# Performance work log

Hardware: AMD Instinct MI355X
Metric: run time of the kernel (lower is better)

Reference implementation:

```python
import jax, jax.numpy as jnp
import numpy as np

EPS = 1e-8  # torch.nn.CosineSimilarity default eps


def setup_inputs() -> dict:
    key = jax.random.key(0)
    k1, k2, k3 = jax.random.split(key, 3)
    B, T, D, L = 16, 256, 512, 32
    v1 = jax.random.normal(k1, (B, T, D), dtype=jnp.float32)
    v1_mask = jnp.ones((B, T), dtype=jnp.float32)
    v2 = jax.random.normal(k2, (B, D), dtype=jnp.float32)
    w = jax.random.normal(k3, (L, D), dtype=jnp.float32)
    return {"v1": v1, "v1_mask": v1_mask, "v2": v2, "w": w}


def reference(v1, v1_mask, v2, w):
    # v1: [B,T,D], v1_mask: [B,T], v2: [B,D], w: [L,D]
    # Original math: cos over D of (w * v1) and (w * v2), per perspective l.
    # Fused: (w_l*a)\cdot(w_l*b) = sum_d w[l,d]^2 a[d] b[d]; likewise for norms.
    v1m = v1 * v1_mask[:, :, None]              # [B,T,D]
    w2 = w * w                                   # [L,D]
    num = jnp.einsum('btd,ld,bd->btl', v1m, w2, v2)          # [B,T,L]
    n1 = jnp.sqrt(jnp.einsum('btd,ld->btl', v1m * v1m, w2))  # [B,T,L]
    n2 = jnp.sqrt(jnp.einsum('bd,ld->bl', v2 * v2, w2))      # [B,L]
    denom = jnp.maximum(n1 * n2[:, None, :], EPS)
    return num / denom                           # [B,T,L]
```

## Files before the change

### kernel.cpp

```cpp
#include <hip/hip_runtime.h>
#include <cstddef>

#define BB      16
#define TDIM    256
#define DDIM    512
#define LDIM    32
#define TROWS   16
#define CD      128
#define NCHUNK  (DDIM / CD)
#define EPSV    1e-8f

__global__ __launch_bounds__(256, 1) void fullmatch_kernel(
    const float* __restrict__ v1,
    const float* __restrict__ v1_mask,
    const float* __restrict__ v2,
    const float* __restrict__ w,
    float* __restrict__ out)
{
    const int tid  = threadIdx.x;
    const int b    = blockIdx.x >> 4;
    const int tgrp = blockIdx.x & 15;
    const int t0b  = tgrp * TROWS;

    const int l  = tid & 31;
    const int tg = tid >> 5;
    const int t0 = t0b + tg * 2;

    __shared__ float v1s[TROWS][CD];
    __shared__ float ws[LDIM][CD + 1];
    __shared__ float hs[LDIM][CD + 1];
    __shared__ float n2s[LDIM];
    __shared__ float red[8][LDIM];

    const float* v2b = v2 + (size_t)b * DDIM;

    {
        const float* wrow = w + (size_t)l * DDIM + tg * 64;
        const float* vseg = v2b + tg * 64;
        float acc = 0.f;
        #pragma unroll 8
        for (int i = 0; i < 64; ++i) {
            const float wv = wrow[i];
            const float vv = vseg[i];
            acc = fmaf(wv * wv, vv * vv, acc);
        }
        red[tg][l] = acc;
    }
    __syncthreads();
    if (tid < LDIM) {
        float s = 0.f;
        #pragma unroll
        for (int i = 0; i < 8; ++i) s += red[i][tid];
        n2s[tid] = sqrtf(s);
    }

    float num0 = 0.f, num1 = 0.f, n1a = 0.f, n1b = 0.f;

    for (int c = 0; c < NCHUNK; ++c) {
        const int d0 = c * CD;
        __syncthreads();

        #pragma unroll
        for (int k = 0; k < 2; ++k) {
            const int f = tid + k * 256;
            const int r = f >> 5;
            const int q = f & 31;
            const float4 val = *(const float4*)(v1 + (size_t)(b * TDIM + t0b + r) * DDIM + d0 + q * 4);
            const float  mk  = v1_mask[b * TDIM + t0b + r];
            float4 o;
            o.x = val.x * mk; o.y = val.y * mk; o.z = val.z * mk; o.w = val.w * mk;
            *(float4*)(&v1s[r][q * 4]) = o;
        }
        #pragma unroll
        for (int k = 0; k < 4; ++k) {
            const int f = tid + k * 256;
            const int r = f >> 5;
            const int q = f & 31;
            const float4 wv = *(const float4*)(w + (size_t)r * DDIM + d0 + q * 4);
            const float4 vv = *(const float4*)(v2b + d0 + q * 4);
            const float w2x = wv.x * wv.x, w2y = wv.y * wv.y, w2z = wv.z * wv.z, w2w = wv.w * wv.w;
            ws[r][q*4+0] = w2x;        ws[r][q*4+1] = w2y;
            ws[r][q*4+2] = w2z;        ws[r][q*4+3] = w2w;
            hs[r][q*4+0] = w2x * vv.x; hs[r][q*4+1] = w2y * vv.y;
            hs[r][q*4+2] = w2z * vv.z; hs[r][q*4+3] = w2w * vv.w;
        }
        __syncthreads();

        const float* __restrict__ a0p = &v1s[tg * 2][0];
        const float* __restrict__ a1p = &v1s[tg * 2 + 1][0];
        const float* __restrict__ wp  = &ws[l][0];
        const float* __restrict__ hp  = &hs[l][0];

        #pragma unroll 8
        for (int dd = 0; dd < CD; dd += 4) {
            const float4 a0 = *(const float4*)(a0p + dd);
            const float4 a1 = *(const float4*)(a1p + dd);
            const float w0 = wp[dd+0], w1 = wp[dd+1], w2_ = wp[dd+2], w3 = wp[dd+3];
            const float h0 = hp[dd+0], h1 = hp[dd+1], h2  = hp[dd+2], h3 = hp[dd+3];

            num0 = fmaf(a0.x, h0, num0);
            num0 = fmaf(a0.y, h1, num0);
            num0 = fmaf(a0.z, h2, num0);
            num0 = fmaf(a0.w, h3, num0);
            num1 = fmaf(a1.x, h0, num1);
            num1 = fmaf(a1.y, h1, num1);
            num1 = fmaf(a1.z, h2, num1);
            num1 = fmaf(a1.w, h3, num1);

            n1a = fmaf(a0.x * a0.x, w0,  n1a);
            n1a = fmaf(a0.y * a0.y, w1,  n1a);
            n1a = fmaf(a0.z * a0.z, w2_, n1a);
            n1a = fmaf(a0.w * a0.w, w3,  n1a);
            n1b = fmaf(a1.x * a1.x, w0,  n1b);
            n1b = fmaf(a1.y * a1.y, w1,  n1b);
            n1b = fmaf(a1.z * a1.z, w2_, n1b);
            n1b = fmaf(a1.w * a1.w, w3,  n1b);
        }
    }

    const float n2v = n2s[l];
    const float den0 = fmaxf(sqrtf(n1a) * n2v, EPSV);
    const float den1 = fmaxf(sqrtf(n1b) * n2v, EPSV);
    out[(size_t)(b * TDIM + t0)     * LDIM + l] = num0 / den0;
    out[(size_t)(b * TDIM + t0 + 1) * LDIM + l] = num1 / den1;
}

extern "C" void kernel_launch(void* const* d_in, const int* in_sizes, int n_in,
                              void* d_out, int out_size, void* d_ws, size_t ws_size,
                              hipStream_t stream) {
    const float* v1      = (const float*)d_in[0];
    const float* v1_mask = (const float*)d_in[1];
    const float* v2      = (const float*)d_in[2];
    const float* w       = (const float*)d_in[3];
    float* out           = (float*)d_out;

    const dim3 grid(BB * (TDIM / TROWS));
    const dim3 block(256);
    fullmatch_kernel<<<grid, block, 0, stream>>>(v1, v1_mask, v2, w, out);
}
```

Measured before the change: 24.25 us.

## Split D across lanes with register-held weights and shuffle reductions

Each 1024-thread block now loads its full 16x512 v1 tile into shared memory once and gives each of the 32 perspectives one wavefront-half. Each lane keeps w^2 and w^2*v2 for its slice of D in registers, accumulates all 16 rows, and then reduces across lanes with xor shuffles. The aim is to drop the chunked shared staging of w and h, the repeated barriers, and the redundant per-block n2 pass, and to write output as coalesced float4 stores. In exchange each thread holds 32 accumulators, and the block does five shuffle rounds per value plus the larger block-size occupancy trade-offs.

```diff
diff --git a/kernel.cpp b/kernel.cpp
--- a/kernel.cpp
+++ b/kernel.cpp
@@ -6,11 +6,10 @@
 #define DDIM    512
 #define LDIM    32
 #define TROWS   16
-#define CD      128
-#define NCHUNK  (DDIM / CD)
+#define NTHREADS 1024
 #define EPSV    1e-8f
 
-__global__ __launch_bounds__(256, 1) void fullmatch_kernel(
+__global__ __launch_bounds__(NTHREADS, 1) void fullmatch_kernel(
     const float* __restrict__ v1,
     const float* __restrict__ v1_mask,
     const float* __restrict__ v2,
@@ -22,107 +21,97 @@
     const int tgrp = blockIdx.x & 15;
     const int t0b  = tgrp * TROWS;
 
-    const int l  = tid & 31;
-    const int tg = tid >> 5;
-    const int t0 = t0b + tg * 2;
+    const int dq = tid & 31;
+    const int l  = tid >> 5;
 
-    __shared__ float v1s[TROWS][CD];
-    __shared__ float ws[LDIM][CD + 1];
-    __shared__ float hs[LDIM][CD + 1];
-    __shared__ float n2s[LDIM];
-    __shared__ float red[8][LDIM];
+    __shared__ float v1s[TROWS][DDIM];
+    __shared__ float otile[TROWS][LDIM];
 
-    const float* v2b = v2 + (size_t)b * DDIM;
-
+    float4 w2r[4], hr[4];
+    float n2p = 0.f;
     {
-        const float* wrow = w + (size_t)l * DDIM + tg * 64;
-        const float* vseg = v2b + tg * 64;
-        float acc = 0.f;
-        #pragma unroll 8
-        for (int i = 0; i < 64; ++i) {
-            const float wv = wrow[i];
-            const float vv = vseg[i];
-            acc = fmaf(wv * wv, vv * vv, acc);
-        }
-        red[tg][l] = acc;
-    }
-    __syncthreads();
-    if (tid < LDIM) {
-        float s = 0.f;
+        const float* __restrict__ wrow = w  + (size_t)l * DDIM;
+        const float* __restrict__ v2b  = v2 + (size_t)b * DDIM;
         #pragma unroll
-        for (int i = 0; i < 8; ++i) s += red[i][tid];
-        n2s[tid] = sqrtf(s);
-    }
-
-    float num0 = 0.f, num1 = 0.f, n1a = 0.f, n1b = 0.f;
-
-    for (int c = 0; c < NCHUNK; ++c) {
-        const int d0 = c * CD;
-        __syncthreads();
-
-        #pragma unroll
-        for (int k = 0; k < 2; ++k) {
-            const int f = tid + k * 256;
-            const int r = f >> 5;
-            const int q = f & 31;
-            const float4 val = *(const float4*)(v1 + (size_t)(b * TDIM + t0b + r) * DDIM + d0 + q * 4);
-            const float  mk  = v1_mask[b * TDIM + t0b + r];
-            float4 o;
-            o.x = val.x * mk; o.y = val.y * mk; o.z = val.z * mk; o.w = val.w * mk;
-            *(float4*)(&v1s[r][q * 4]) = o;
-        }
-        #pragma unroll
-        for (int k = 0; k < 4; ++k) {
-            const int f = tid + k * 256;
-            const int r = f >> 5;
-            const int q = f & 31;
-            const float4 wv = *(const float4*)(w + (size_t)r * DDIM + d0 + q * 4);
-            const float4 vv = *(const float4*)(v2b + d0 + q * 4);
-            const float w2x = wv.x * wv.x, w2y = wv.y * wv.y, w2z = wv.z * wv.z, w2w = wv.w * wv.w;
-            ws[r][q*4+0] = w2x;        ws[r][q*4+1] = w2y;
-            ws[r][q*4+2] = w2z;        ws[r][q*4+3] = w2w;
-            hs[r][q*4+0] = w2x * vv.x; hs[r][q*4+1] = w2y * vv.y;
-            hs[r][q*4+2] = w2z * vv.z; hs[r][q*4+3] = w2w * vv.w;
-        }
-        __syncthreads();
-
-        const float* __restrict__ a0p = &v1s[tg * 2][0];
-        const float* __restrict__ a1p = &v1s[tg * 2 + 1][0];
-        const float* __restrict__ wp  = &ws[l][0];
-        const float* __restrict__ hp  = &hs[l][0];
-
-        #pragma unroll 8
-        for (int dd = 0; dd < CD; dd += 4) {
-            const float4 a0 = *(const float4*)(a0p + dd);
-            const float4 a1 = *(const float4*)(a1p + dd);
-            const float w0 = wp[dd+0], w1 = wp[dd+1], w2_ = wp[dd+2], w3 = wp[dd+3];
-            const float h0 = hp[dd+0], h1 = hp[dd+1], h2  = hp[dd+2], h3 = hp[dd+3];
-
-            num0 = fmaf(a0.x, h0, num0);
-            num0 = fmaf(a0.y, h1, num0);
-            num0 = fmaf(a0.z, h2, num0);
-            num0 = fmaf(a0.w, h3, num0);
-            num1 = fmaf(a1.x, h0, num1);
-            num1 = fmaf(a1.y, h1, num1);
-            num1 = fmaf(a1.z, h2, num1);
-            num1 = fmaf(a1.w, h3, num1);
-
-            n1a = fmaf(a0.x * a0.x, w0,  n1a);
-            n1a = fmaf(a0.y * a0.y, w1,  n1a);
-            n1a = fmaf(a0.z * a0.z, w2_, n1a);
-            n1a = fmaf(a0.w * a0.w, w3,  n1a);
-            n1b = fmaf(a1.x * a1.x, w0,  n1b);
-            n1b = fmaf(a1.y * a1.y, w1,  n1b);
-            n1b = fmaf(a1.z * a1.z, w2_, n1b);
-            n1b = fmaf(a1.w * a1.w, w3,  n1b);
+        for (int j = 0; j < 4; ++j) {
+            const int d = dq * 4 + j * 128;
+            const float4 wv = *(const float4*)(wrow + d);
+            const float4 vv = *(const float4*)(v2b + d);
+            float4 w2;
+            w2.x = wv.x * wv.x; w2.y = wv.y * wv.y;
+            w2.z = wv.z * wv.z; w2.w = wv.w * wv.w;
+            w2r[j] = w2;
+            float4 h;
+            h.x = w2.x * vv.x; h.y = w2.y * vv.y;
+            h.z = w2.z * vv.z; h.w = w2.w * vv.w;
+            hr[j] = h;
+            n2p = fmaf(h.x, vv.x, n2p);
+            n2p = fmaf(h.y, vv.y, n2p);
+            n2p = fmaf(h.z, vv.z, n2p);
+            n2p = fmaf(h.w, vv.w, n2p);
         }
     }
 
-    const float n2v = n2s[l];
-    const float den0 = fmaxf(sqrtf(n1a) * n2v, EPSV);
-    const float den1 = fmaxf(sqrtf(n1b) * n2v, EPSV);
-    out[(size_t)(b * TDIM + t0)     * LDIM + l] = num0 / den0;
-    out[(size_t)(b * TDIM + t0 + 1) * LDIM + l] = num1 / den1;
+    #pragma unroll
+    for (int k = 0; k < 2; ++k) {
+        const int f = tid + k * NTHREADS;
+        const int r = f >> 7;
+        const int q = f & 127;
+        const float4 val = *(const float4*)(v1 + (size_t)(b * TDIM + t0b + r) * DDIM + q * 4);
+        const float  mk  = v1_mask[b * TDIM + t0b + r];
+        float4 o;
+        o.x = val.x * mk; o.y = val.y * mk; o.z = val.z * mk; o.w = val.w * mk;
+        *(float4*)(&v1s[r][q * 4]) = o;
+    }
+    __syncthreads();
+
+    float accN[TROWS], accD[TROWS];
+    #pragma unroll
+    for (int t = 0; t < TROWS; ++t) { accN[t] = 0.f; accD[t] = 0.f; }
+
+    #pragma unroll
+    for (int j = 0; j < 4; ++j) {
+        const float4 w2 = w2r[j];
+        const float4 h  = hr[j];
+        const float* __restrict__ base = &v1s[0][dq * 4 + j * 128];
+        #pragma unroll
+        for (int t = 0; t < TROWS; ++t) {
+            const float4 a = *(const float4*)(base + t * DDIM);
+            accN[t] = fmaf(a.x, h.x, accN[t]);
+            accN[t] = fmaf(a.y, h.y, accN[t]);
+            accN[t] = fmaf(a.z, h.z, accN[t]);
+            accN[t] = fmaf(a.w, h.w, accN[t]);
+            accD[t] = fmaf(a.x * a.x, w2.x, accD[t]);
+            accD[t] = fmaf(a.y * a.y, w2.y, accD[t]);
+            accD[t] = fmaf(a.z * a.z, w2.z, accD[t]);
+            accD[t] = fmaf(a.w * a.w, w2.w, accD[t]);
+        }
+    }
+
+    #pragma unroll
+    for (int m = 16; m >= 1; m >>= 1) {
+        n2p += __shfl_xor(n2p, m, 64);
+        #pragma unroll
+        for (int t = 0; t < TROWS; ++t) {
+            accN[t] += __shfl_xor(accN[t], m, 64);
+            accD[t] += __shfl_xor(accD[t], m, 64);
+        }
+    }
+
+    if (dq == 0) {
+        const float n2v = sqrtf(n2p);
+        #pragma unroll
+        for (int t = 0; t < TROWS; ++t) {
+            const float den = fmaxf(sqrtf(accD[t]) * n2v, EPSV);
+            otile[t][l] = accN[t] / den;
+        }
+    }
+    __syncthreads();
+
+    if (tid < (TROWS * LDIM) / 4) {
+        const size_t base = (size_t)(b * TDIM + t0b) * LDIM;
+        *(float4*)(out + base + tid * 4) = *(const float4*)(&otile[0][0] + tid * 4);
+    }
 }
 
 extern "C" void kernel_launch(void* const* d_in, const int* in_sizes, int n_in,
@@ -135,6 +124,6 @@
     float* out           = (float*)d_out;
 
     const dim3 grid(BB * (TDIM / TROWS));
-    const dim3 block(256);
+    const dim3 block(NTHREADS);
     fullmatch_kernel<<<grid, block, 0, stream>>>(v1, v1_mask, v2, w, out);
 }
```

Result: faster. 21.73 us (-10.4%).
